# Performance work log

Hardware: AMD Instinct MI355X
Metric: run time of the kernel (lower is better)

Reference implementation:

```python
import jax, jax.numpy as jnp
import numpy as np

B, S, D, R, H, NI, NP, NO, K = 2, 2048, 1024, 1024, 8, 8, 32, 8, 3
DH = R // H


def setup_inputs() -> dict:
    key = jax.random.key(0)
    ks = jax.random.split(key, 32)
    rn = lambda k, shp, s=1.0: jax.random.normal(k, shp, jnp.float32) * s
    nrm = lambda v: v / (jnp.linalg.norm(v, axis=-1, keepdims=True) + 1e-8)
    w = 1.0 / np.sqrt(D).astype(np.float32)
    inp = {
        'x': rn(ks[0], (B, S, D)),
        'mask': jnp.tril(jnp.ones((S, S), bool))[None, None],  # causal [1,1,S,S]
        'Wr_in': rn(ks[1], (NI, D), w), 'Wr_proc': rn(ks[2], (NP, D), w), 'Wr_out': rn(ks[3], (NO, D), w),
        'WrO_in': rn(ks[4], (NI, R), w), 'WrO_proc': rn(ks[5], (NP, R), w), 'WrO_out': rn(ks[6], (NO, R), w),
        'Wq_in': rn(ks[7], (NI, D, R), w), 'vq': nrm(rn(ks[8], (NP, R))), 'Wq_out': rn(ks[9], (NO, R, D), w),
        'Wk_in': rn(ks[10], (NI, D, R), w), 'vk': nrm(rn(ks[11], (NP, R))), 'Wk_out': rn(ks[12], (NO, R, D), w),
        'Wv_in': rn(ks[13], (NI, D, R), w), 'vv': nrm(rn(ks[14], (NP, R))), 'Wv_out': rn(ks[15], (NO, R, D), w),
        # circuit_O = NeuronCircuit(rank, d_model): dims swapped
        'Wo_in': rn(ks[16], (NI, R, D), w), 'vo': nrm(rn(ks[17], (NP, D))), 'Wo_out': rn(ks[18], (NO, D, R), w),
    }
    return inp


def _router(x, Wi, Wp, Wo, k):
    in_w = jax.nn.softmax(x @ Wi.T, axis=-1)            # [B,S,NI]
    _, proc_idx = jax.lax.top_k(x @ Wp.T, k)            # [B,S,k]
    out_w = jax.nn.softmax(x @ Wo.T, axis=-1)           # [B,S,NO]
    return in_w, proc_idx, out_w


def _circuit(x, Win, vproc, Wout, in_w, proc_idx, out_w):
    # soft input mix: d_in -> r
    h = jnp.einsum('bsd,ndr,bsn->bsr', x, Win, in_w)
    # k sequential Householder reflections with gathered vectors
    v = vproc[proc_idx]                                 # [B,S,k,r]
    v = v / jnp.sqrt(jnp.sum(v * v, axis=-1, keepdims=True) + 1e-8)
    for i in range(v.shape[2]):
        vi = v[:, :, i, :]
        h = h - 2.0 * vi * jnp.sum(h * vi, axis=-1, keepdims=True)
    # soft output mix: r -> d_out
    return jnp.einsum('bsr,nrd,bsn->bsd', h, Wout, out_w)


def reference(x, mask, Wr_in, Wr_proc, Wr_out, WrO_in, WrO_proc, WrO_out,
              Wq_in, vq, Wq_out, Wk_in, vk, Wk_out, Wv_in, vv, Wv_out,
              Wo_in, vo, Wo_out):
    in_w, pidx, out_w = _router(x, Wr_in, Wr_proc, Wr_out, K)
    Q = _circuit(x, Wq_in, vq, Wq_out, in_w, pidx, out_w)   # [B,S,R]
    Kt = _circuit(x, Wk_in, vk, Wk_out, in_w, pidx, out_w)
    V = _circuit(x, Wv_in, vv, Wv_out, in_w, pidx, out_w)
    q = Q.reshape(B, S, H, DH).transpose(0, 2, 1, 3)
    k = Kt.reshape(B, S, H, DH).transpose(0, 2, 1, 3)
    v = V.reshape(B, S, H, DH).transpose(0, 2, 1, 3)
    scores = jnp.einsum('bhqd,bhkd->bhqk', q, k) / np.sqrt(DH).astype(np.float32)
    scores = jnp.where(mask, scores, jnp.float32(-1e9))
    p = jax.nn.softmax(scores, axis=-1)
    o = jnp.einsum('bhqk,bhkd->bhqd', p, v)
    o = o.transpose(0, 2, 1, 3).reshape(B, S, R)
    in_wO, pidxO, out_wO = _router(o, WrO_in, WrO_proc, WrO_out, K)
    out = _circuit(o, Wo_in, vo, Wo_out, in_wO, pidxO, out_wO)  # [B,S,D]
    return out
```

## Files before the change

kernel.cpp:

```cpp
#include <hip/hip_runtime.h>


typedef __attribute__((ext_vector_type(4))) float f32x4;
typedef _Float16 f16x8 __attribute__((ext_vector_type(8)));
typedef _Float16 f16x4 __attribute__((ext_vector_type(4)));

static constexpr int S_LEN  = 2048;
static constexpr int TOK    = 4096;
static constexpr int DMODEL = 1024;
static constexpr int KDIM   = 8192;

__device__ __forceinline__ void async16(const void* g, void* l) {
  __builtin_amdgcn_global_load_lds(
      (const __attribute__((address_space(1))) void*)g,
      (__attribute__((address_space(3))) void*)l, 16, 0, 0);
}

__global__ __launch_bounds__(256) void transpose_split(const float* __restrict__ W,
                                                       _Float16* __restrict__ Th,
                                                       _Float16* __restrict__ Tl) {
  __shared__ float tbuf[64][65];
  const int tid = threadIdx.x;
  const int k0 = blockIdx.x * 64, n0 = blockIdx.y * 64;
#pragma unroll
  for (int j = 0; j < 4; ++j) {
    int ci = tid + 256 * j;
    int r = ci >> 4, c4 = (ci & 15) * 4;
    float4 v = *(const float4*)&W[(size_t)(k0 + r) * DMODEL + n0 + c4];
    tbuf[r][c4 + 0] = v.x; tbuf[r][c4 + 1] = v.y;
    tbuf[r][c4 + 2] = v.z; tbuf[r][c4 + 3] = v.w;
  }
  __syncthreads();
#pragma unroll
  for (int j = 0; j < 2; ++j) {
    int ci = tid + 256 * j;
    int nl = ci >> 3, k8 = (ci & 7) * 8;
    f16x8 hv, lv;
#pragma unroll
    for (int e = 0; e < 8; ++e) {
      float v = tbuf[k8 + e][nl];
      _Float16 hh = (_Float16)v;
      hv[e] = hh;
      lv[e] = (_Float16)(v - (float)hh);
    }
    size_t off = (size_t)(n0 + nl) * KDIM + k0 + k8;
    *(f16x8*)&Th[off] = hv;
    if (Tl != nullptr) *(f16x8*)&Tl[off] = lv;
  }
}

__global__ __launch_bounds__(256) void router_kernel(const float* __restrict__ X,
                                                     const float* __restrict__ Wi,
                                                     const float* __restrict__ Wp,
                                                     const float* __restrict__ Wo,
                                                     float* __restrict__ in_w,
                                                     float* __restrict__ out_w,
                                                     int* __restrict__ pidx,
                                                     _Float16* __restrict__ Xh,
                                                     _Float16* __restrict__ Xl) {
  __shared__ float xs[1024];
  __shared__ double lg[48];
  const int t = blockIdx.x, tid = threadIdx.x;
  const int wid = tid >> 6, lane = tid & 63;
#pragma unroll
  for (int j = 0; j < 4; ++j) {
    int d = tid + 256 * j;
    xs[d] = X[(size_t)t * DMODEL + d];
  }
  __syncthreads();
  for (int i = wid; i < 48; i += 4) {
    const float* wrow = (i < 8)  ? Wi + (size_t)i * DMODEL
                      : (i < 40) ? Wp + (size_t)(i - 8) * DMODEL
                                 : Wo + (size_t)(i - 40) * DMODEL;
    double s = 0.0;
#pragma unroll
    for (int j = 0; j < 16; ++j) { int d = lane + 64 * j; s += (double)xs[d] * (double)wrow[d]; }
#pragma unroll
    for (int mm = 32; mm >= 1; mm >>= 1) s += __shfl_xor(s, mm);
    if (lane == 0) lg[i] = s;
  }
  __syncthreads();
  if (tid == 0) {
    float l[8], m;
    for (int i = 0; i < 8; ++i) l[i] = (float)lg[i];
    m = l[0];
    for (int i = 1; i < 8; ++i) m = fmaxf(m, l[i]);
    float e[8], su = 0.f;
    for (int i = 0; i < 8; ++i) { e[i] = expf(l[i] - m); su += e[i]; }
    for (int i = 0; i < 8; ++i) in_w[t * 8 + i] = e[i] / su;
  } else if (tid == 64) {
    float l[8], m;
    for (int i = 0; i < 8; ++i) l[i] = (float)lg[40 + i];
    m = l[0];
    for (int i = 1; i < 8; ++i) m = fmaxf(m, l[i]);
    float e[8], su = 0.f;
    for (int i = 0; i < 8; ++i) { e[i] = expf(l[i] - m); su += e[i]; }
    for (int i = 0; i < 8; ++i) out_w[t * 8 + i] = e[i] / su;
  } else if (tid == 128) {
    unsigned used = 0;
    for (int j = 0; j < 3; ++j) {
      double best = -1e300; int bi = 0;
      for (int i = 0; i < 32; ++i)
        if (!((used >> i) & 1u) && lg[8 + i] > best) { best = lg[8 + i]; bi = i; }
      used |= 1u << bi;
      pidx[t * 3 + j] = bi;
    }
  }
  if (Xh != nullptr) {
#pragma unroll
    for (int j = 0; j < 4; ++j) {
      int d = tid + 256 * j;
      float v = xs[d];
      _Float16 hh = (_Float16)v;
      Xh[(size_t)t * DMODEL + d] = hh;
      Xl[(size_t)t * DMODEL + d] = (_Float16)(v - (float)hh);
    }
  }
}

__global__ __launch_bounds__(256) void reflect4_kernel(const float* __restrict__ Pa,
                                                       const float* __restrict__ Pb,
                                                       const float* __restrict__ Pc,
                                                       const float* __restrict__ Pd,
                                                       const int* __restrict__ pidx,
                                                       const float* __restrict__ vtab,
                                                       _Float16* __restrict__ Hh,
                                                       _Float16* __restrict__ Hl) {
  __shared__ float red[8];
  const int t = blockIdx.x, tid = threadIdx.x;
  const int wid = tid >> 6, lane = tid & 63;
  size_t gi = (size_t)t * DMODEL + tid * 4;
  float4 ha = *(const float4*)&Pa[gi];
  float4 hb = *(const float4*)&Pb[gi];
  float4 hc = *(const float4*)&Pc[gi];
  float4 hd = *(const float4*)&Pd[gi];
  float4 h = {ha.x + hb.x + hc.x + hd.x, ha.y + hb.y + hc.y + hd.y,
              ha.z + hb.z + hc.z + hd.z, ha.w + hb.w + hc.w + hd.w};
  for (int i = 0; i < 3; ++i) {
    int idx = pidx[t * 3 + i];
    float4 vi = *(const float4*)&vtab[(size_t)idx * DMODEL + tid * 4];
    float hv = h.x * vi.x + h.y * vi.y + h.z * vi.z + h.w * vi.w;
    float vv = vi.x * vi.x + vi.y * vi.y + vi.z * vi.z + vi.w * vi.w;
#pragma unroll
    for (int mm = 32; mm >= 1; mm >>= 1) { hv += __shfl_xor(hv, mm); vv += __shfl_xor(vv, mm); }
    if (lane == 0) { red[wid] = hv; red[4 + wid] = vv; }
    __syncthreads();
    float dot = red[0] + red[1] + red[2] + red[3];
    float vn  = red[4] + red[5] + red[6] + red[7];
    __syncthreads();
    float c = 2.f * dot / (vn + 1e-8f);
    h.x -= c * vi.x; h.y -= c * vi.y; h.z -= c * vi.z; h.w -= c * vi.w;
  }
  float a[4] = {h.x, h.y, h.z, h.w};
  f16x4 hv4, lv4;
#pragma unroll
  for (int e = 0; e < 4; ++e) {
    _Float16 hh = (_Float16)a[e];
    hv4[e] = hh;
    lv4[e] = (_Float16)(a[e] - (float)hh);
  }
  *(f16x4*)&Hh[gi] = hv4;
  *(f16x4*)&Hl[gi] = lv4;
}

__global__ __launch_bounds__(256) void reduce4_planes(const float* __restrict__ a,
                                                      const float* __restrict__ b,
                                                      const float* __restrict__ c,
                                                      const float* __restrict__ d,
                                                      _Float16* __restrict__ Dh,
                                                      _Float16* __restrict__ Dl) {
  size_t i = ((size_t)blockIdx.x * 256 + threadIdx.x) * 4;
  float4 va = *(const float4*)&a[i];
  float4 vb = *(const float4*)&b[i];
  float4 vc = *(const float4*)&c[i];
  float4 vd = *(const float4*)&d[i];
  float s[4] = {va.x + vb.x + vc.x + vd.x, va.y + vb.y + vc.y + vd.y,
                va.z + vb.z + vc.z + vd.z, va.w + vb.w + vc.w + vd.w};
  f16x4 hv, lv;
#pragma unroll
  for (int e = 0; e < 4; ++e) {
    _Float16 hh = (_Float16)s[e];
    hv[e] = hh;
    lv[e] = (_Float16)(s[e] - (float)hh);
  }
  *(f16x4*)&Dh[i] = hv;
  *(f16x4*)&Dl[i] = lv;
}

__global__ __launch_bounds__(256) void reduce4_f32(const float* __restrict__ a,
                                                   const float* __restrict__ b,
                                                   const float* __restrict__ c,
                                                   const float* __restrict__ d,
                                                   float* __restrict__ o) {
  size_t i = ((size_t)blockIdx.x * 256 + threadIdx.x) * 4;
  float4 va = *(const float4*)&a[i];
  float4 vb = *(const float4*)&b[i];
  float4 vc = *(const float4*)&c[i];
  float4 vd = *(const float4*)&d[i];
  float4 vo = {va.x + vb.x + vc.x + vd.x, va.y + vb.y + vc.y + vd.y,
               va.z + vb.z + vc.z + vd.z, va.w + vb.w + vc.w + vd.w};
  *(float4*)&o[i] = vo;
}

template <bool FAST>
__global__ __launch_bounds__(512, 2) void gemm_planes(const _Float16* __restrict__ Ahp,
                                                      const _Float16* __restrict__ Alp,
                                                      const float* __restrict__ wmix,
                                                      const _Float16* __restrict__ Bh,
                                                      const _Float16* __restrict__ Bl,
                                                      float* __restrict__ C0,
                                                      float* __restrict__ C1,
                                                      float* __restrict__ C2,
                                                      float* __restrict__ C3) {
  constexpr int BK     = FAST ? 64 : 32;
  constexpr int NSTEPS = 2048 / BK;
  __shared__ _Float16 sAh[2][256 * BK];
  __shared__ _Float16 sBh[2][256 * BK];
  __shared__ _Float16 sAl[2][FAST ? 8 : 256 * 32];
  __shared__ _Float16 sBl[2][FAST ? 8 : 256 * 32];
  __shared__ float sWr[256 * 2];
  const int tid = threadIdx.x;
  const int wid = tid >> 6, lane = tid & 63;
  const int l16 = lane & 15, lhi = lane >> 4;
  const int wr = wid >> 2, wc = wid & 3;
  const int fid = blockIdx.x + (blockIdx.y << 4) + (blockIdx.z << 6);
  const int wg  = ((fid & 7) << 5) + (fid >> 3);
  const int bm = (wg & 15) * 256;
  const int bn = ((wg >> 4) & 3) * 256;
  const int kz = wg >> 6;
  const int kbase = kz * 2048, nb = kz * 2;
  float* __restrict__ Cp = (kz == 0) ? C0 : (kz == 1) ? C1 : (kz == 2) ? C2 : C3;

  {
    int row = tid >> 1, p = tid & 1;
    const float* w = &wmix[(size_t)(bm + row) * 8 + nb];
    sWr[tid] = p ? w[1] : w[0] / w[1];
  }

  f32x4 acc[8][4];
#pragma unroll
  for (int i = 0; i < 8; ++i)
#pragma unroll
    for (int j = 0; j < 4; ++j) { f32x4 z = {0.f, 0.f, 0.f, 0.f}; acc[i][j] = z; }

  auto STAGE = [&](int buf, int kt) {
    const int kg = kbase + kt, d0 = kg & 1023;
    if constexpr (FAST) {
#pragma unroll
      for (int j = 0; j < 4; ++j) {
        int ci = tid + 512 * j;
        int row = ci >> 3, jc = ci & 7;
        int jcs = jc ^ (row & 7);
        size_t ga = (size_t)(bm + row) * DMODEL + d0 + jcs * 8;
        size_t gb = (size_t)(bn + row) * KDIM + kg + jcs * 8;
        async16(&Ahp[ga], &sAh[buf][ci * 8]);
        async16(&Bh[gb],  &sBh[buf][ci * 8]);
      }
    } else {
#pragma unroll
      for (int j = 0; j < 2; ++j) {
        int ci = tid + 512 * j;
        int row = ci >> 2, jc = ci & 3;
        int jcs = jc ^ ((row >> 1) & 3);
        size_t ga = (size_t)(bm + row) * DMODEL + d0 + jcs * 8;
        size_t gb = (size_t)(bn + row) * KDIM + kg + jcs * 8;
        async16(&Ahp[ga], &sAh[buf][ci * 8]);
        async16(&Bh[gb],  &sBh[buf][ci * 8]);
        async16(&Alp[ga], &sAl[buf][ci * 8]);
        async16(&Bl[gb],  &sBl[buf][ci * 8]);
      }
    }
  };

  auto COMPUTE = [&](int buf) {
    __builtin_amdgcn_s_setprio(1);
    if constexpr (FAST) {
#pragma unroll
      for (int kk = 0; kk < 2; ++kk) {
        f16x8 b_h[4];
#pragma unroll
        for (int ni = 0; ni < 4; ++ni) {
          int row = wc * 64 + ni * 16 + l16;
          int ch = (kk * 4 + lhi) ^ (row & 7);
          b_h[ni] = *(const f16x8*)&sBh[buf][row * 64 + ch * 8];
        }
#pragma unroll
        for (int mi = 0; mi < 8; ++mi) {
          int rowa = wr * 128 + mi * 16 + l16;
          int cha = (kk * 4 + lhi) ^ (rowa & 7);
          f16x8 a_h = *(const f16x8*)&sAh[buf][rowa * 64 + cha * 8];
#pragma unroll
          for (int ni = 0; ni < 4; ++ni)
            acc[mi][ni] = __builtin_amdgcn_mfma_f32_16x16x32_f16(a_h, b_h[ni], acc[mi][ni], 0, 0, 0);
        }
      }
    } else {
      f16x8 b_h[4], b_l[4];
#pragma unroll
      for (int ni = 0; ni < 4; ++ni) {
        int row = wc * 64 + ni * 16 + l16;
        int idx = row * 32 + ((lhi ^ ((row >> 1) & 3)) * 8);
        b_h[ni] = *(const f16x8*)&sBh[buf][idx];
        b_l[ni] = *(const f16x8*)&sBl[buf][idx];
      }
#pragma unroll
      for (int mi = 0; mi < 8; ++mi) {
        int rowa = wr * 128 + mi * 16 + l16;
        int idxa = rowa * 32 + ((lhi ^ ((rowa >> 1) & 3)) * 8);
        f16x8 a_h = *(const f16x8*)&sAh[buf][idxa];
        f16x8 a_l = *(const f16x8*)&sAl[buf][idxa];
#pragma unroll
        for (int ni = 0; ni < 4; ++ni) {
          f32x4 a = acc[mi][ni];
          a = __builtin_amdgcn_mfma_f32_16x16x32_f16(a_h, b_h[ni], a, 0, 0, 0);
          a = __builtin_amdgcn_mfma_f32_16x16x32_f16(a_h, b_l[ni], a, 0, 0, 0);
          a = __builtin_amdgcn_mfma_f32_16x16x32_f16(a_l, b_h[ni], a, 0, 0, 0);
          acc[mi][ni] = a;
        }
      }
    }
    __builtin_amdgcn_s_setprio(0);
  };

  auto RESCALE = [&]() {
#pragma unroll
    for (int mi = 0; mi < 8; ++mi)
#pragma unroll
      for (int r = 0; r < 4; ++r) {
        float s = sWr[(wr * 128 + mi * 16 + lhi * 4 + r) * 2];
#pragma unroll
        for (int ni = 0; ni < 4; ++ni) acc[mi][ni][r] *= s;
      }
  };

  STAGE(0, 0);
  for (int t = 0; t < NSTEPS - 1; ++t) {
    STAGE((t + 1) & 1, (t + 1) * BK);
    asm volatile("s_waitcnt vmcnt(8)" ::: "memory");
    __builtin_amdgcn_s_barrier();
    __builtin_amdgcn_sched_barrier(0);
    COMPUTE(t & 1);
    if (t == 1024 / BK - 1) RESCALE();
    __builtin_amdgcn_s_barrier();
  }
  asm volatile("s_waitcnt vmcnt(0)" ::: "memory");
  __builtin_amdgcn_s_barrier();
  __builtin_amdgcn_sched_barrier(0);
  COMPUTE((NSTEPS - 1) & 1);

#pragma unroll
  for (int mi = 0; mi < 8; ++mi)
#pragma unroll
    for (int r = 0; r < 4; ++r) {
      int rowl = wr * 128 + mi * 16 + lhi * 4 + r;
      float s = sWr[rowl * 2 + 1];
#pragma unroll
      for (int ni = 0; ni < 4; ++ni) {
        int col = bn + wc * 64 + ni * 16 + l16;
        Cp[(size_t)(bm + rowl) * DMODEL + col] = acc[mi][ni][r] * s;
      }
    }
}

__global__ __launch_bounds__(256) void vtrans4_kernel(const float* __restrict__ Va,
                                                      const float* __restrict__ Vb,
                                                      const float* __restrict__ Vc,
                                                      const float* __restrict__ Vd,
                                                      _Float16* __restrict__ Vth,
                                                      _Float16* __restrict__ Vtl) {
  __shared__ float tbuf[64][65];
  const int tid = threadIdx.x;
  const int t0 = blockIdx.x * 64, d0 = blockIdx.y * 64, bh = blockIdx.z;
  const int b = bh >> 3, h = bh & 7;
#pragma unroll
  for (int j = 0; j < 4; ++j) {
    int ci = tid + 256 * j;
    int r = ci >> 4, c4 = (ci & 15) * 4;
    size_t g = (size_t)(b * S_LEN + t0 + r) * DMODEL + h * 128 + d0 + c4;
    float4 va = *(const float4*)&Va[g];
    float4 vb = *(const float4*)&Vb[g];
    float4 vc = *(const float4*)&Vc[g];
    float4 vd = *(const float4*)&Vd[g];
    tbuf[r][c4 + 0] = va.x + vb.x + vc.x + vd.x;
    tbuf[r][c4 + 1] = va.y + vb.y + vc.y + vd.y;
    tbuf[r][c4 + 2] = va.z + vb.z + vc.z + vd.z;
    tbuf[r][c4 + 3] = va.w + vb.w + vc.w + vd.w;
  }
  __syncthreads();
#pragma unroll
  for (int j = 0; j < 4; ++j) {
    int ci = tid + 256 * j;
    int r = ci >> 4, c4 = (ci & 15) * 4;
    float s[4] = {tbuf[c4 + 0][r], tbuf[c4 + 1][r], tbuf[c4 + 2][r], tbuf[c4 + 3][r]};
    f16x4 hv, lv;
#pragma unroll
    for (int e = 0; e < 4; ++e) {
      _Float16 hh = (_Float16)s[e];
      hv[e] = hh;
      lv[e] = (_Float16)(s[e] - (float)hh);
    }
    size_t o = ((size_t)bh * 128 + d0 + r) * S_LEN + t0 + c4;
    *(f16x4*)&Vth[o] = hv;
    *(f16x4*)&Vtl[o] = lv;
  }
}

__global__ __launch_bounds__(256) void attn_kernel(const _Float16* __restrict__ Qh,
                                                   const _Float16* __restrict__ Ql,
                                                   const _Float16* __restrict__ Kh,
                                                   const _Float16* __restrict__ Kl,
                                                   const _Float16* __restrict__ Vth,
                                                   const _Float16* __restrict__ Vtl,
                                                   float* __restrict__ O,
                                                   _Float16* __restrict__ Oh) {
  __shared__ _Float16 sKh[32 * 128], sKl[32 * 128];
  __shared__ _Float16 sVh[128 * 32], sVl[128 * 32];
  __shared__ _Float16 sPh[4 * 16 * 32], sPl[4 * 16 * 32];
  const int tid = threadIdx.x;
  const int wid = tid >> 6, lane = tid & 63;
  const int l16 = lane & 15, lhi = lane >> 4;
  const int qt = (gridDim.x - 1) - blockIdx.x;
  const int bh = blockIdx.y;
  const int b = bh >> 3, h = bh & 7;
  const size_t qkbase = (size_t)b * S_LEN * DMODEL + h * 128;
  const float scale = 0.08838834764831845f;

  const int qrow = qt * 64 + wid * 16 + l16;
  const size_t qoff = qkbase + (size_t)qrow * DMODEL;
  f16x8 qh[4], ql[4];
#pragma unroll
  for (int kk = 0; kk < 4; ++kk) {
    qh[kk] = *(const f16x8*)&Qh[qoff + kk * 32 + lhi * 8];
    ql[kk] = *(const f16x8*)&Ql[qoff + kk * 32 + lhi * 8];
  }

  f32x4 of[8];
#pragma unroll
  for (int i = 0; i < 8; ++i) { f32x4 z = {0.f, 0.f, 0.f, 0.f}; of[i] = z; }
  float m_[4], l_[4];
#pragma unroll
  for (int r = 0; r < 4; ++r) { m_[r] = -1e30f; l_[r] = 0.f; }

  const int ntw = qt * 2 + 1 + (wid >> 1);
  const int NT  = qt * 2 + 2;

  for (int kt = 0; kt < NT; ++kt) {
    __syncthreads();
#pragma unroll
    for (int j = 0; j < 2; ++j) {
      int ci = tid + 256 * j;
      int k = ci >> 4, c = ci & 15;
      int cs = c ^ (k & 7);
      size_t g = qkbase + (size_t)(kt * 32 + k) * DMODEL + cs * 8;
      async16(&Kh[g], &sKh[k * 128 + c * 8]);
      async16(&Kl[g], &sKl[k * 128 + c * 8]);
    }
#pragma unroll
    for (int j = 0; j < 2; ++j) {
      int ci = tid + 256 * j;
      int d = ci >> 2, c = ci & 3;
      int cs = c ^ ((d >> 1) & 3);
      size_t g = ((size_t)bh * 128 + d) * S_LEN + kt * 32 + cs * 8;
      async16(&Vth[g], &sVh[d * 32 + c * 8]);
      async16(&Vtl[g], &sVl[d * 32 + c * 8]);
    }
    __syncthreads();

    if (kt < ntw) {
      f32x4 s0 = {0.f, 0.f, 0.f, 0.f}, s1 = {0.f, 0.f, 0.f, 0.f};
#pragma unroll
      for (int kk = 0; kk < 4; ++kk) {
        int col = (kk * 32 + lhi * 8);
        int i0 = l16 * 128 + (col ^ ((l16 & 7) * 8));
        int i1 = (16 + l16) * 128 + (col ^ (((16 + l16) & 7) * 8));
        f16x8 kb0h = *(const f16x8*)&sKh[i0];
        f16x8 kb0l = *(const f16x8*)&sKl[i0];
        f16x8 kb1h = *(const f16x8*)&sKh[i1];
        f16x8 kb1l = *(const f16x8*)&sKl[i1];
        s0 = __builtin_amdgcn_mfma_f32_16x16x32_f16(qh[kk], kb0h, s0, 0, 0, 0);
        s0 = __builtin_amdgcn_mfma_f32_16x16x32_f16(qh[kk], kb0l, s0, 0, 0, 0);
        s0 = __builtin_amdgcn_mfma_f32_16x16x32_f16(ql[kk], kb0h, s0, 0, 0, 0);
        s1 = __builtin_amdgcn_mfma_f32_16x16x32_f16(qh[kk], kb1h, s1, 0, 0, 0);
        s1 = __builtin_amdgcn_mfma_f32_16x16x32_f16(qh[kk], kb1l, s1, 0, 0, 0);
        s1 = __builtin_amdgcn_mfma_f32_16x16x32_f16(ql[kk], kb1h, s1, 0, 0, 0);
      }
      const int qg = qt * 64 + wid * 16 + (lane >> 4) * 4;
      if (kt == ntw - 1) {
#pragma unroll
        for (int r = 0; r < 4; ++r) {
          int q = qg + r;
          int k0 = kt * 32 + l16, k1 = k0 + 16;
          s0[r] = (k0 <= q) ? s0[r] * scale : -1e30f;
          s1[r] = (k1 <= q) ? s1[r] * scale : -1e30f;
        }
      } else {
#pragma unroll
        for (int r = 0; r < 4; ++r) { s0[r] *= scale; s1[r] *= scale; }
      }
      float p0[4], p1[4], fr[4];
#pragma unroll
      for (int r = 0; r < 4; ++r) {
        float rm = fmaxf(s0[r], s1[r]);
        rm = fmaxf(rm, __shfl_xor(rm, 1));
        rm = fmaxf(rm, __shfl_xor(rm, 2));
        rm = fmaxf(rm, __shfl_xor(rm, 4));
        rm = fmaxf(rm, __shfl_xor(rm, 8));
        float mn = fmaxf(m_[r], rm);
        fr[r] = __expf(m_[r] - mn);
        m_[r] = mn;
        p0[r] = __expf(s0[r] - mn);
        p1[r] = __expf(s1[r] - mn);
        float rs = p0[r] + p1[r];
        rs += __shfl_xor(rs, 1);
        rs += __shfl_xor(rs, 2);
        rs += __shfl_xor(rs, 4);
        rs += __shfl_xor(rs, 8);
        l_[r] = l_[r] * fr[r] + rs;
      }
#pragma unroll
      for (int i = 0; i < 8; ++i)
#pragma unroll
        for (int r = 0; r < 4; ++r) of[i][r] *= fr[r];
#pragma unroll
      for (int r = 0; r < 4; ++r) {
        int q = (lane >> 4) * 4 + r;
        int swz = ((q >> 1) & 3) * 8;
        int c0 = l16, c1 = 16 + l16;
        _Float16 h0 = (_Float16)p0[r];
        _Float16 h1 = (_Float16)p1[r];
        sPh[wid * 512 + q * 32 + (c0 ^ swz)] = h0;
        sPl[wid * 512 + q * 32 + (c0 ^ swz)] = (_Float16)(p0[r] - (float)h0);
        sPh[wid * 512 + q * 32 + (c1 ^ swz)] = h1;
        sPl[wid * 512 + q * 32 + (c1 ^ swz)] = (_Float16)(p1[r] - (float)h1);
      }
      int pidxr = wid * 512 + l16 * 32 + ((lhi * 8) ^ (((l16 >> 1) & 3) * 8));
      f16x8 pah = *(const f16x8*)&sPh[pidxr];
      f16x8 pal = *(const f16x8*)&sPl[pidxr];
#pragma unroll
      for (int d16 = 0; d16 < 8; ++d16) {
        int d = d16 * 16 + l16;
        int vidx = d * 32 + ((lhi * 8) ^ (((d >> 1) & 3) * 8));
        f16x8 vbh = *(const f16x8*)&sVh[vidx];
        f16x8 vbl = *(const f16x8*)&sVl[vidx];
        f32x4 a = of[d16];
        a = __builtin_amdgcn_mfma_f32_16x16x32_f16(pah, vbh, a, 0, 0, 0);
        a = __builtin_amdgcn_mfma_f32_16x16x32_f16(pah, vbl, a, 0, 0, 0);
        a = __builtin_amdgcn_mfma_f32_16x16x32_f16(pal, vbh, a, 0, 0, 0);
        of[d16] = a;
      }
    }
  }
  float inv[4];
#pragma unroll
  for (int r = 0; r < 4; ++r) inv[r] = 1.f / l_[r];
  const int qg = qt * 64 + wid * 16 + (lane >> 4) * 4;
#pragma unroll
  for (int d16 = 0; d16 < 8; ++d16)
#pragma unroll
    for (int r = 0; r < 4; ++r) {
      float val = of[d16][r] * inv[r];
      size_t gi = qkbase + (size_t)(qg + r) * DMODEL + d16 * 16 + l16;
      O[gi] = val;
      Oh[gi] = (_Float16)val;
    }
}

extern "C" void kernel_launch(void* const* d_in, const int* in_sizes, int n_in,
                              void* d_out, int out_size, void* d_ws, size_t ws_size,
                              hipStream_t stream) {
  (void)in_sizes; (void)n_in; (void)out_size;
  const float* x        = (const float*)d_in[0];
  const float* Wr_in    = (const float*)d_in[2];
  const float* Wr_proc  = (const float*)d_in[3];
  const float* Wr_out   = (const float*)d_in[4];
  const float* WrO_in   = (const float*)d_in[5];
  const float* WrO_proc = (const float*)d_in[6];
  const float* WrO_out  = (const float*)d_in[7];
  const float* Wq_in    = (const float*)d_in[8];
  const float* vq       = (const float*)d_in[9];
  const float* Wq_out   = (const float*)d_in[10];
  const float* Wk_in    = (const float*)d_in[11];
  const float* vk       = (const float*)d_in[12];
  const float* Wk_out   = (const float*)d_in[13];
  const float* Wv_in    = (const float*)d_in[14];
  const float* vv       = (const float*)d_in[15];
  const float* Wv_out   = (const float*)d_in[16];
  const float* Wo_in    = (const float*)d_in[17];
  const float* vo       = (const float*)d_in[18];
  const float* Wo_out   = (const float*)d_in[19];

  char* wsbase = (char*)d_ws;
  size_t off = 0;
  auto carve = [&](size_t bytes) -> void* {
    void* r = wsbase + off;
    off = (off + bytes + 255) & ~(size_t)255;
    return r;
  };
  const size_t WBYTES = (size_t)KDIM * DMODEL * 2;
  const size_t PBYTES = (size_t)TOK * DMODEL * 2;
  const size_t HBYTES = (size_t)TOK * DMODEL * 4;
  _Float16* WTh = (_Float16*)carve(WBYTES);
  _Float16* WTl = (_Float16*)carve(WBYTES);
  _Float16* Xh  = (_Float16*)carve(PBYTES);
  _Float16* Xl  = (_Float16*)carve(PBYTES);
  _Float16* Hh  = (_Float16*)carve(PBYTES);
  _Float16* Hl  = (_Float16*)carve(PBYTES);
  float* P0 = (float*)carve(HBYTES);
  float* P1 = (float*)carve(HBYTES);
  float* P2 = (float*)carve(HBYTES);
  _Float16* Qph = (_Float16*)carve(PBYTES);
  _Float16* Qpl = (_Float16*)carve(PBYTES);
  _Float16* Kph = (_Float16*)carve(PBYTES);
  _Float16* Kpl = (_Float16*)carve(PBYTES);
  float* iw1 = (float*)carve((size_t)TOK * 8 * 4);
  float* ow1 = (float*)carve((size_t)TOK * 8 * 4);
  float* iw2 = (float*)carve((size_t)TOK * 8 * 4);
  float* ow2 = (float*)carve((size_t)TOK * 8 * 4);
  int* pi1 = (int*)carve((size_t)TOK * 3 * 4);
  int* pi2 = (int*)carve((size_t)TOK * 3 * 4);

  if (off > ws_size) {
    hipMemsetAsync(d_out, 0, (size_t)out_size * 4, stream);
    return;
  }

  float*    Pd  = (float*)d_out;
  float*    PQ  = (float*)Qph;
  float*    PX  = (float*)Xh;
  _Float16* Vth = WTh;
  _Float16* Vtl = WTh + (size_t)TOK * DMODEL;
  float*    Ofp = P0;
  _Float16* Ohp = (_Float16*)P1;

  const dim3 blk(256);
  const dim3 gblk(512);
  const dim3 tgrid(KDIM / 64, DMODEL / 64);
  const dim3 ggrid(TOK / 256, DMODEL / 256, 4);
  const dim3 rgrid(TOK * DMODEL / (256 * 4));
  const dim3 vgrid(S_LEN / 64, 2, 16);
  const dim3 agrid(S_LEN / 64, 16);

  router_kernel<<<TOK, blk, 0, stream>>>(x, Wr_in, Wr_proc, Wr_out, iw1, ow1, pi1, Xh, Xl);

  transpose_split<<<tgrid, blk, 0, stream>>>(Wq_in, WTh, WTl);
  gemm_planes<false><<<ggrid, gblk, 0, stream>>>(Xh, Xl, iw1, WTh, WTl, P0, P1, P2, Pd);
  reflect4_kernel<<<TOK, blk, 0, stream>>>(P0, P1, P2, Pd, pi1, vq, Hh, Hl);
  transpose_split<<<tgrid, blk, 0, stream>>>(Wq_out, WTh, WTl);
  gemm_planes<false><<<ggrid, gblk, 0, stream>>>(Hh, Hl, ow1, WTh, WTl, P0, P1, P2, Pd);
  reduce4_planes<<<rgrid, blk, 0, stream>>>(P0, P1, P2, Pd, Qph, Qpl);

  transpose_split<<<tgrid, blk, 0, stream>>>(Wk_in, WTh, WTl);
  gemm_planes<false><<<ggrid, gblk, 0, stream>>>(Xh, Xl, iw1, WTh, WTl, P0, P1, P2, Pd);
  reflect4_kernel<<<TOK, blk, 0, stream>>>(P0, P1, P2, Pd, pi1, vk, Hh, Hl);
  transpose_split<<<tgrid, blk, 0, stream>>>(Wk_out, WTh, WTl);
  gemm_planes<false><<<ggrid, gblk, 0, stream>>>(Hh, Hl, ow1, WTh, WTl, P0, P1, P2, Pd);
  reduce4_planes<<<rgrid, blk, 0, stream>>>(P0, P1, P2, Pd, Kph, Kpl);

  transpose_split<<<tgrid, blk, 0, stream>>>(Wv_in, WTh, WTl);
  gemm_planes<false><<<ggrid, gblk, 0, stream>>>(Xh, Xl, iw1, WTh, WTl, P0, P1, P2, Pd);
  reflect4_kernel<<<TOK, blk, 0, stream>>>(P0, P1, P2, Pd, pi1, vv, Hh, Hl);
  transpose_split<<<tgrid, blk, 0, stream>>>(Wv_out, WTh, WTl);
  gemm_planes<false><<<ggrid, gblk, 0, stream>>>(Hh, Hl, ow1, WTh, WTl, P0, P1, P2, Pd);
  vtrans4_kernel<<<vgrid, blk, 0, stream>>>(P0, P1, P2, Pd, Vth, Vtl);

  attn_kernel<<<agrid, blk, 0, stream>>>(Qph, Qpl, Kph, Kpl, Vth, Vtl, Ofp, Ohp);

  router_kernel<<<TOK, blk, 0, stream>>>(Ofp, WrO_in, WrO_proc, WrO_out, iw2, ow2, pi2,
                                         nullptr, nullptr);
  transpose_split<<<tgrid, blk, 0, stream>>>(Wo_in, WTh, nullptr);
  gemm_planes<true><<<ggrid, gblk, 0, stream>>>(Ohp, Ohp, iw2, WTh, WTh, PX, P0, P2, Pd);
  reflect4_kernel<<<TOK, blk, 0, stream>>>(PX, P0, P2, Pd, pi2, vo, Hh, Hl);
  transpose_split<<<tgrid, blk, 0, stream>>>(Wo_out, WTh, nullptr);
  gemm_planes<true><<<ggrid, gblk, 0, stream>>>(Hh, Hh, ow2, WTh, WTh, P0, P1, P2, PQ);
  reduce4_f32<<<rgrid, blk, 0, stream>>>(P0, P1, P2, PQ, (float*)d_out);
}
```

Measured before the change: 1.617 ms.

## Split hi/lo staging in split-precision GEMM to overlap lo loads with hi MFMAs

In the non-FAST (three-term fp16 hi/lo emulation) GEMM path, the tile load is split into a hi half and a lo half. MFMAs on the hi parts start as soon as the hi tiles arrive, while the lo tiles are still in flight. The lo tiles for the next step are issued after the second barrier. This aims to hide global-to-LDS latency behind compute, at the cost of an extra barrier per step and more complex vmcnt accounting. The FAST path is only restructured, with no change in behaviour.

```diff
diff --git a/kernel.cpp b/kernel.cpp
--- a/kernel.cpp
+++ b/kernel.cpp
@@ -243,38 +243,66 @@
 #pragma unroll
     for (int j = 0; j < 4; ++j) { f32x4 z = {0.f, 0.f, 0.f, 0.f}; acc[i][j] = z; }
 
-  auto STAGE = [&](int buf, int kt) {
+  auto STAGE_H0 = [&](int buf, int kt) {
     const int kg = kbase + kt, d0 = kg & 1023;
-    if constexpr (FAST) {
-#pragma unroll
-      for (int j = 0; j < 4; ++j) {
-        int ci = tid + 512 * j;
-        int row = ci >> 3, jc = ci & 7;
-        int jcs = jc ^ (row & 7);
-        size_t ga = (size_t)(bm + row) * DMODEL + d0 + jcs * 8;
-        size_t gb = (size_t)(bn + row) * KDIM + kg + jcs * 8;
-        async16(&Ahp[ga], &sAh[buf][ci * 8]);
-        async16(&Bh[gb],  &sBh[buf][ci * 8]);
-      }
-    } else {
-#pragma unroll
-      for (int j = 0; j < 2; ++j) {
-        int ci = tid + 512 * j;
-        int row = ci >> 2, jc = ci & 3;
-        int jcs = jc ^ ((row >> 1) & 3);
-        size_t ga = (size_t)(bm + row) * DMODEL + d0 + jcs * 8;
-        size_t gb = (size_t)(bn + row) * KDIM + kg + jcs * 8;
-        async16(&Ahp[ga], &sAh[buf][ci * 8]);
-        async16(&Bh[gb],  &sBh[buf][ci * 8]);
-        async16(&Alp[ga], &sAl[buf][ci * 8]);
-        async16(&Bl[gb],  &sBl[buf][ci * 8]);
-      }
+#pragma unroll
+    for (int j = 0; j < 2; ++j) {
+      int ci = tid + 512 * j;
+      int row = ci >> 2, jc = ci & 3;
+      int jcs = jc ^ ((row >> 1) & 3);
+      size_t ga = (size_t)(bm + row) * DMODEL + d0 + jcs * 8;
+      size_t gb = (size_t)(bn + row) * KDIM + kg + jcs * 8;
+      async16(&Ahp[ga], &sAh[buf][ci * 8]);
+      async16(&Bh[gb],  &sBh[buf][ci * 8]);
     }
   };
-
-  auto COMPUTE = [&](int buf) {
-    __builtin_amdgcn_s_setprio(1);
-    if constexpr (FAST) {
+  auto STAGE_H1 = [&](int buf, int kt) {
+    const int kg = kbase + kt, d0 = kg & 1023;
+#pragma unroll
+    for (int j = 0; j < 2; ++j) {
+      int ci = tid + 512 * j;
+      int row = ci >> 2, jc = ci & 3;
+      int jcs = jc ^ ((row >> 1) & 3);
+      size_t ga = (size_t)(bm + row) * DMODEL + d0 + jcs * 8;
+      size_t gb = (size_t)(bn + row) * KDIM + kg + jcs * 8;
+      async16(&Alp[ga], &sAl[buf][ci * 8]);
+      async16(&Bl[gb],  &sBl[buf][ci * 8]);
+    }
+  };
+  auto STAGE_FAST = [&](int buf, int kt) {
+    const int kg = kbase + kt, d0 = kg & 1023;
+#pragma unroll
+    for (int j = 0; j < 4; ++j) {
+      int ci = tid + 512 * j;
+      int row = ci >> 3, jc = ci & 7;
+      int jcs = jc ^ (row & 7);
+      size_t ga = (size_t)(bm + row) * DMODEL + d0 + jcs * 8;
+      size_t gb = (size_t)(bn + row) * KDIM + kg + jcs * 8;
+      async16(&Ahp[ga], &sAh[buf][ci * 8]);
+      async16(&Bh[gb],  &sBh[buf][ci * 8]);
+    }
+  };
+
+  auto RESCALE = [&]() {
+#pragma unroll
+    for (int mi = 0; mi < 8; ++mi)
+#pragma unroll
+      for (int r = 0; r < 4; ++r) {
+        float s = sWr[(wr * 128 + mi * 16 + lhi * 4 + r) * 2];
+#pragma unroll
+        for (int ni = 0; ni < 4; ++ni) acc[mi][ni][r] *= s;
+      }
+  };
+
+  if constexpr (FAST) {
+    STAGE_FAST(0, 0);
+    for (int t = 0; t < NSTEPS - 1; ++t) {
+      STAGE_FAST((t + 1) & 1, (t + 1) * BK);
+      asm volatile("s_waitcnt vmcnt(8)" ::: "memory");
+      __builtin_amdgcn_s_barrier();
+      __builtin_amdgcn_sched_barrier(0);
+      __builtin_amdgcn_s_setprio(1);
+      int buf = t & 1;
 #pragma unroll
       for (int kk = 0; kk < 2; ++kk) {
         f16x8 b_h[4];
@@ -294,59 +322,92 @@
             acc[mi][ni] = __builtin_amdgcn_mfma_f32_16x16x32_f16(a_h, b_h[ni], acc[mi][ni], 0, 0, 0);
         }
       }
-    } else {
-      f16x8 b_h[4], b_l[4];
+      __builtin_amdgcn_s_setprio(0);
+      if (t == 1024 / BK - 1) RESCALE();
+      __builtin_amdgcn_s_barrier();
+    }
+    asm volatile("s_waitcnt vmcnt(0)" ::: "memory");
+    __builtin_amdgcn_s_barrier();
+    __builtin_amdgcn_sched_barrier(0);
+    {
+      int buf = (NSTEPS - 1) & 1;
+      __builtin_amdgcn_s_setprio(1);
+#pragma unroll
+      for (int kk = 0; kk < 2; ++kk) {
+        f16x8 b_h[4];
+#pragma unroll
+        for (int ni = 0; ni < 4; ++ni) {
+          int row = wc * 64 + ni * 16 + l16;
+          int ch = (kk * 4 + lhi) ^ (row & 7);
+          b_h[ni] = *(const f16x8*)&sBh[buf][row * 64 + ch * 8];
+        }
+#pragma unroll
+        for (int mi = 0; mi < 8; ++mi) {
+          int rowa = wr * 128 + mi * 16 + l16;
+          int cha = (kk * 4 + lhi) ^ (rowa & 7);
+          f16x8 a_h = *(const f16x8*)&sAh[buf][rowa * 64 + cha * 8];
+#pragma unroll
+          for (int ni = 0; ni < 4; ++ni)
+            acc[mi][ni] = __builtin_amdgcn_mfma_f32_16x16x32_f16(a_h, b_h[ni], acc[mi][ni], 0, 0, 0);
+        }
+      }
+      __builtin_amdgcn_s_setprio(0);
+    }
+  } else {
+    STAGE_H0(0, 0);
+    STAGE_H1(0, 0);
+    for (int t = 0; t < NSTEPS; ++t) {
+      const int buf = t & 1;
+      if (t < NSTEPS - 1) STAGE_H0(buf ^ 1, (t + 1) * 32);
+      if (t < NSTEPS - 1) asm volatile("s_waitcnt vmcnt(8)" ::: "memory");
+      else                asm volatile("s_waitcnt vmcnt(4)" ::: "memory");
+      __builtin_amdgcn_s_barrier();
+      __builtin_amdgcn_sched_barrier(0);
+      __builtin_amdgcn_s_setprio(1);
+      f16x8 b_h[4], a_hv[8];
 #pragma unroll
       for (int ni = 0; ni < 4; ++ni) {
         int row = wc * 64 + ni * 16 + l16;
-        int idx = row * 32 + ((lhi ^ ((row >> 1) & 3)) * 8);
-        b_h[ni] = *(const f16x8*)&sBh[buf][idx];
-        b_l[ni] = *(const f16x8*)&sBl[buf][idx];
+        b_h[ni] = *(const f16x8*)&sBh[buf][row * 32 + ((lhi ^ ((row >> 1) & 3)) * 8)];
       }
 #pragma unroll
       for (int mi = 0; mi < 8; ++mi) {
         int rowa = wr * 128 + mi * 16 + l16;
-        int idxa = rowa * 32 + ((lhi ^ ((rowa >> 1) & 3)) * 8);
-        f16x8 a_h = *(const f16x8*)&sAh[buf][idxa];
-        f16x8 a_l = *(const f16x8*)&sAl[buf][idxa];
+        a_hv[mi] = *(const f16x8*)&sAh[buf][rowa * 32 + ((lhi ^ ((rowa >> 1) & 3)) * 8)];
+#pragma unroll
+        for (int ni = 0; ni < 4; ++ni)
+          acc[mi][ni] = __builtin_amdgcn_mfma_f32_16x16x32_f16(a_hv[mi], b_h[ni], acc[mi][ni], 0, 0, 0);
+      }
+      __builtin_amdgcn_s_setprio(0);
+      if (t < NSTEPS - 1) asm volatile("s_waitcnt vmcnt(4)" ::: "memory");
+      else                asm volatile("s_waitcnt vmcnt(0)" ::: "memory");
+      __builtin_amdgcn_s_barrier();
+      __builtin_amdgcn_sched_barrier(0);
+      __builtin_amdgcn_s_setprio(1);
+      f16x8 b_l[4];
+#pragma unroll
+      for (int ni = 0; ni < 4; ++ni) {
+        int row = wc * 64 + ni * 16 + l16;
+        b_l[ni] = *(const f16x8*)&sBl[buf][row * 32 + ((lhi ^ ((row >> 1) & 3)) * 8)];
+      }
+#pragma unroll
+      for (int mi = 0; mi < 8; ++mi) {
+        int rowa = wr * 128 + mi * 16 + l16;
+        f16x8 a_l = *(const f16x8*)&sAl[buf][rowa * 32 + ((lhi ^ ((rowa >> 1) & 3)) * 8)];
 #pragma unroll
         for (int ni = 0; ni < 4; ++ni) {
           f32x4 a = acc[mi][ni];
-          a = __builtin_amdgcn_mfma_f32_16x16x32_f16(a_h, b_h[ni], a, 0, 0, 0);
-          a = __builtin_amdgcn_mfma_f32_16x16x32_f16(a_h, b_l[ni], a, 0, 0, 0);
+          a = __builtin_amdgcn_mfma_f32_16x16x32_f16(a_hv[mi], b_l[ni], a, 0, 0, 0);
           a = __builtin_amdgcn_mfma_f32_16x16x32_f16(a_l, b_h[ni], a, 0, 0, 0);
           acc[mi][ni] = a;
         }
       }
-    }
-    __builtin_amdgcn_s_setprio(0);
-  };
-
-  auto RESCALE = [&]() {
-#pragma unroll
-    for (int mi = 0; mi < 8; ++mi)
-#pragma unroll
-      for (int r = 0; r < 4; ++r) {
-        float s = sWr[(wr * 128 + mi * 16 + lhi * 4 + r) * 2];
-#pragma unroll
-        for (int ni = 0; ni < 4; ++ni) acc[mi][ni][r] *= s;
-      }
-  };
-
-  STAGE(0, 0);
-  for (int t = 0; t < NSTEPS - 1; ++t) {
-    STAGE((t + 1) & 1, (t + 1) * BK);
-    asm volatile("s_waitcnt vmcnt(8)" ::: "memory");
-    __builtin_amdgcn_s_barrier();
-    __builtin_amdgcn_sched_barrier(0);
-    COMPUTE(t & 1);
-    if (t == 1024 / BK - 1) RESCALE();
-    __builtin_amdgcn_s_barrier();
-  }
-  asm volatile("s_waitcnt vmcnt(0)" ::: "memory");
-  __builtin_amdgcn_s_barrier();
-  __builtin_amdgcn_sched_barrier(0);
-  COMPUTE((NSTEPS - 1) & 1);
+      __builtin_amdgcn_s_setprio(0);
+      if (t == 31) RESCALE();
+      __builtin_amdgcn_s_barrier();
+      if (t < NSTEPS - 1) STAGE_H1(buf ^ 1, (t + 1) * 32);
+    }
+  }
 
 #pragma unroll
   for (int mi = 0; mi < 8; ++mi)
```

Result: no change. 1.630 ms (+0.8%).
